# Kernel optimization log

Measured on AMD Instinct MI355X. Metric: run time of the kernel, lower is better.

## Reference

```python
import jax, jax.numpy as jnp
import numpy as np

TEMPERATURE = 0.07
NEG = -1e9  # finite stand-in for -inf; exp(-1e9) underflows to 0 in fp32, identical math


def setup_inputs() -> dict:
    key = jax.random.key(0)
    k1, k2 = jax.random.split(key)
    B, D = 8192, 128
    emb = jax.random.normal(k1, (B, D), dtype=jnp.float32)
    emb = emb / jnp.linalg.norm(emb, axis=1, keepdims=True)  # docstring: normalized embeddings
    labels = jax.random.randint(k2, (B,), 0, 2048, dtype=jnp.int64)
    return {"embeddings": emb, "labels": labels}


def reference(embeddings, labels):
    B = labels.shape[0]
    # [B, B] pairwise similarities / temperature
    sim = jnp.matmul(embeddings, embeddings.T) / TEMPERATURE
    eye = jnp.eye(B, dtype=bool)
    sim = jnp.where(eye, NEG, sim)  # mask self-similarity
    # positives: same outfit id, excluding self
    pos_mask = (labels[None, :] == labels[:, None]) & (~eye)
    # row-wise log-softmax (torch code does log_softmax over each row)
    log_probs = jax.nn.log_softmax(sim, axis=1)
    pos_count = jnp.sum(pos_mask, axis=1)  # [B]
    pos_sum = jnp.sum(jnp.where(pos_mask, log_probs, 0.0), axis=1)  # [B]
    has_pos = pos_count > 0
    row_mean = jnp.where(has_pos, pos_sum / jnp.maximum(pos_count, 1), 0.0)
    count = jnp.sum(has_pos)
    loss = -jnp.sum(row_mean) / jnp.maximum(count, 1)
    return loss
```

## Files before the change

### kernel.cpp

```cpp
#include <hip/hip_runtime.h>


#define BATCH 8192
#define DIMK  128
#define INV_T 14.285714285714286f
#define MSUB  14.285714285714286f
#define K1    20.609929155311264f
#define K2    20.609929155311264f

typedef short bf16x8 __attribute__((ext_vector_type(8)));
typedef float f32x4  __attribute__((ext_vector_type(4)));

__device__ __forceinline__ unsigned short f2bf_rne(float f) {
    unsigned u = __float_as_uint(f);
    u += 0x7FFFu + ((u >> 16) & 1u);
    return (unsigned short)(u >> 16);
}
__device__ __forceinline__ float bf2f(unsigned short b) {
    return __uint_as_float(((unsigned)b) << 16);
}

__global__ __launch_bounds__(256) void
prep_kernel(const float* __restrict__ emb, const int* __restrict__ labels,
            ushort* __restrict__ Ebf, float* __restrict__ gsum, int* __restrict__ gcnt,
            float4* __restrict__ zzero) {
    if (blockIdx.x < 1024) {
        int i = blockIdx.x * 256 + threadIdx.x;
        if (i < 67584) {
            float4 z = {0.f, 0.f, 0.f, 0.f};
            zzero[i] = z;
        }
        float4 v = ((const float4*)emb)[i];
        ushort4 o;
        o.x = f2bf_rne(v.x); o.y = f2bf_rne(v.y);
        o.z = f2bf_rne(v.z); o.w = f2bf_rne(v.w);
        ((ushort4*)Ebf)[i] = o;
    } else {
        __shared__ int labs[BATCH];
        const int tid = threadIdx.x;
#pragma unroll
        for (int it = 0; it < 8; ++it)
            ((int4*)labs)[it * 256 + tid] = ((const int4*)labels)[it * 256 + tid];
        __syncthreads();

        const int lane = tid & 63;
        const int wid  = tid >> 6;
        const int c    = (blockIdx.x - 1024) * 4 + wid;
        float2 acc = {0.f, 0.f};
        int cnt = 0;
        int nl = labs[lane];
        for (int j0 = 0; j0 < BATCH; j0 += 64) {
            int cur = nl;
            int nidx = j0 + 64 < BATCH ? j0 + 64 : 0;
            nl = labs[nidx + lane];
            unsigned long long m = __ballot(cur == c);
            cnt += __popcll(m);
            while (m) {
                int j = __ffsll(m) - 1;
                m &= m - 1;
                float2 v = *(const float2*)(emb + (size_t)(j0 + j) * DIMK + lane * 2);
                acc.x += v.x; acc.y += v.y;
            }
        }
        *(float2*)(gsum + (size_t)c * DIMK + lane * 2) = acc;
        if (lane == 0) gcnt[c] = cnt;
    }
}

__global__ __launch_bounds__(256) void
contrastive_main(const ushort* __restrict__ Ebf, float* __restrict__ zpartR,
                 float* __restrict__ zcol) {
    __shared__ __align__(16) ushort Bs[2048 * 8];
    __shared__ float cpart[4][256];
    const int tid  = threadIdx.x;
    const int lane = tid & 63;
    const int wid  = tid >> 6;
    const int quad = lane >> 4;
    const int l16  = lane & 15;

    int b = blockIdx.x >> 1;
    const int half = blockIdx.x & 1;
    int ti = 0;
    while (b >= 32 - ti) { b -= 32 - ti; ++ti; }
    const int tj = ti + b;
    const int row_base = ti * 256 + half * 128 + wid * 32;

    bf16x8 afrag[2][4];
#pragma unroll
    for (int mt = 0; mt < 2; ++mt)
#pragma unroll
        for (int kk = 0; kk < 4; ++kk)
            afrag[mt][kk] = *(const bf16x8*)(Ebf + (size_t)(row_base + mt * 16 + l16) * DIMK
                                             + kk * 32 + quad * 8);

    float zacc[8];
#pragma unroll
    for (int s = 0; s < 8; ++s) zacc[s] = 0.f;

#pragma unroll
    for (int phase = 0; phase < 2; ++phase) {
        const int col_base = tj * 256 + phase * 128;
        __syncthreads();
#pragma unroll
        for (int it = 0; it < 8; ++it) {
            int f   = it * 256 + tid;
            int col = f >> 4;
            int c   = f & 15;
            uint4 v = *(const uint4*)(Ebf + (size_t)(col_base + col) * DIMK + c * 8);
            *(uint4*)&Bs[((col >> 4) * 256 + c * 16 + ((col & 15) ^ c)) * 8] = v;
        }
        __syncthreads();

        for (int nt = 0; nt < 8; ++nt) {
            bf16x8 bfrag[4];
#pragma unroll
            for (int kk = 0; kk < 4; ++kk) {
                const int c2 = kk * 4 + quad;
                bfrag[kk] = *(const bf16x8*)&Bs[(nt * 256 + c2 * 16 + (l16 ^ c2)) * 8];
            }

            float csum = 0.f;
#pragma unroll
            for (int mt = 0; mt < 2; ++mt) {
                f32x4 c = {0.f, 0.f, 0.f, 0.f};
#pragma unroll
                for (int kk = 0; kk < 4; ++kk)
                    c = __builtin_amdgcn_mfma_f32_16x16x32_bf16(afrag[mt][kk], bfrag[kk], c, 0, 0, 0);
#pragma unroll
                for (int r = 0; r < 4; ++r) {
                    float e = __builtin_amdgcn_exp2f(__builtin_fmaf(c[r], K1, -K2));
                    zacc[mt * 4 + r] += e;
                    csum += e;
                }
            }
            csum += __shfl_xor(csum, 16, 64);
            csum += __shfl_xor(csum, 32, 64);
            if (quad == 0) cpart[wid][phase * 128 + nt * 16 + l16] = csum;
        }
    }

#pragma unroll
    for (int s = 0; s < 8; ++s) {
        float z = zacc[s];
#pragma unroll
        for (int m = 1; m <= 8; m <<= 1) z += __shfl_xor(z, m, 64);
        if (l16 == 0) {
            int row = row_base + (s >> 2) * 16 + quad * 4 + (s & 3);
            zpartR[(size_t)tj * BATCH + row] = z;
        }
    }

    __syncthreads();
    if (ti != tj) {
        float s = cpart[0][tid] + cpart[1][tid] + cpart[2][tid] + cpart[3][tid];
        atomicAdd(&zcol[tj * 256 + tid], s);
    }
}

__global__ __launch_bounds__(256) void
finalize1(const float* __restrict__ emb, const ushort* __restrict__ Ebf,
          const int* __restrict__ labels, const float* __restrict__ gsum,
          const int* __restrict__ gcnt, const float* __restrict__ zpartR,
          const float* __restrict__ zcol,
          float* __restrict__ bpart, int* __restrict__ bcnt) {
    __shared__ float sf[4];
    __shared__ int   si[4];
    const int lane = threadIdx.x & 63;
    const int wid  = threadIdx.x >> 6;

    float wsum = 0.f;
    int   wcnt = 0;
#pragma unroll
    for (int it = 0; it < 4; ++it) {
        const int r   = blockIdx.x * 16 + wid * 4 + it;
        const int lab = labels[r];
        const int P   = gcnt[lab] - 1;

        float2 ev = *(const float2*)(emb  + (size_t)r   * DIMK + lane * 2);
        float2 gv = *(const float2*)(gsum + (size_t)lab * DIMK + lane * 2);
        unsigned bb = *(const unsigned*)(Ebf + (size_t)r * DIMK + lane * 2);
        float b0 = bf2f((unsigned short)(bb & 0xFFFF));
        float b1 = bf2f((unsigned short)(bb >> 16));

        float dotg = ev.x * gv.x + ev.y * gv.y;
        float ssd  = ev.x * ev.x + ev.y * ev.y;
        float sdbf = b0 * b0 + b1 * b1;
        float Z = 0.f;
        if (lane < 32)       Z = zpartR[(size_t)lane * BATCH + r];
        else if (lane == 32) Z = zcol[r];

#pragma unroll
        for (int m = 1; m <= 32; m <<= 1) {
            dotg += __shfl_xor(dotg, m, 64);
            ssd  += __shfl_xor(ssd,  m, 64);
            sdbf += __shfl_xor(sdbf, m, 64);
            Z    += __shfl_xor(Z,    m, 64);
        }
        Z -= __builtin_amdgcn_exp2f(__builtin_fmaf(sdbf, K1, -K2));

        const bool has = (P > 0);
        wsum += has ? ((dotg - ssd) * INV_T / (float)P - MSUB - __logf(Z)) : 0.f;
        wcnt += has ? 1 : 0;
    }

    if (lane == 0) { sf[wid] = wsum; si[wid] = wcnt; }
    __syncthreads();
    if (threadIdx.x == 0) {
        bpart[blockIdx.x] = sf[0] + sf[1] + sf[2] + sf[3];
        bcnt [blockIdx.x] = si[0] + si[1] + si[2] + si[3];
    }
}

__global__ __launch_bounds__(256) void
finalize2(const float* __restrict__ bpart, const int* __restrict__ bcnt,
          float* __restrict__ out) {
    __shared__ float sf[4];
    __shared__ int   si[4];
    const int t = threadIdx.x;
    float v = 0.f; int c = 0;
#pragma unroll
    for (int k = 0; k < 2; ++k) {
        v += bpart[t + k * 256];
        c += bcnt [t + k * 256];
    }
#pragma unroll
    for (int m = 1; m <= 32; m <<= 1) {
        v += __shfl_xor(v, m, 64);
        c += __shfl_xor(c, m, 64);
    }
    if ((t & 63) == 0) { sf[t >> 6] = v; si[t >> 6] = c; }
    __syncthreads();
    if (t == 0) {
        float tot = sf[0] + sf[1] + sf[2] + sf[3];
        int cc = si[0] + si[1] + si[2] + si[3];
        out[0] = -tot / (float)(cc > 0 ? cc : 1);
    }
}

extern "C" void kernel_launch(void* const* d_in, const int* in_sizes, int n_in,
                              void* d_out, int out_size, void* d_ws, size_t ws_size,
                              hipStream_t stream) {
    const float* emb  = (const float*)d_in[0];
    const int* labels = (const int*)d_in[1];
    float* out        = (float*)d_out;

    char* ws = (char*)d_ws;
    ushort* Ebf    = (ushort*)ws;
    float*  zpartR = (float*)(ws + (2u << 20));
    float*  zcol   = (float*)(ws + (3u << 20));
    float*  gsum   = (float*)(ws + (4u << 20));
    int*    gcnt   = (int*)  (ws + (5u << 20));
    float*  bpart  = (float*)(ws + (5u << 20) + 8192);
    int*    bcnt   = (int*)  (ws + (5u << 20) + 16384);

    prep_kernel<<<1536, 256, 0, stream>>>(emb, labels, Ebf, gsum, gcnt, (float4*)zpartR);
    contrastive_main<<<1056, 256, 0, stream>>>(Ebf, zpartR, zcol);
    finalize1<<<512, 256, 0, stream>>>(emb, Ebf, labels, gsum, gcnt, zpartR, zcol, bpart, bcnt);
    finalize2<<<1, 256, 0, stream>>>(bpart, bcnt, out);
}
```

Before: 101.3 us.

## Double-buffer B tiles via direct global-to-LDS loads, use 32x32 MFMA, fuse final reduction

The main kernel now stages column chunks of 64 rows into two LDS buffers with global_load_lds and explicit vmcnt waits, so loading the next chunk overlaps MFMA and exp work on the current one. It also switches from 16x16x32 to 32x32x16 bf16 MFMA, which changes fragment layout and the row/column reduction mapping. The separate finalize2 launch is removed: the last block of finalize1, found with an atomic ticket, does the final sum. The risks are the hand-written waitcnt/barrier ordering and higher register use from the 16-wide accumulators.

```diff
diff --git a/kernel.cpp b/kernel.cpp
--- a/kernel.cpp
+++ b/kernel.cpp
@@ -9,7 +9,7 @@
 #define K2    20.609929155311264f
 
 typedef short bf16x8 __attribute__((ext_vector_type(8)));
-typedef float f32x4  __attribute__((ext_vector_type(4)));
+typedef float f32x16 __attribute__((ext_vector_type(16)));
 
 __device__ __forceinline__ unsigned short f2bf_rne(float f) {
     unsigned u = __float_as_uint(f);
@@ -20,11 +20,18 @@
     return __uint_as_float(((unsigned)b) << 16);
 }
 
+__device__ __forceinline__ void gload16(const ushort* g, ushort* l) {
+    __builtin_amdgcn_global_load_lds(
+        (const __attribute__((address_space(1))) void*)g,
+        (__attribute__((address_space(3))) void*)l, 16, 0, 0);
+}
+
 __global__ __launch_bounds__(256) void
 prep_kernel(const float* __restrict__ emb, const int* __restrict__ labels,
             ushort* __restrict__ Ebf, float* __restrict__ gsum, int* __restrict__ gcnt,
-            float4* __restrict__ zzero) {
+            float4* __restrict__ zzero, int* __restrict__ ticket) {
     if (blockIdx.x < 1024) {
+        if (blockIdx.x == 0 && threadIdx.x == 0) *ticket = 0;
         int i = blockIdx.x * 256 + threadIdx.x;
         if (i < 67584) {
             float4 z = {0.f, 0.f, 0.f, 0.f};
@@ -70,13 +77,13 @@
 __global__ __launch_bounds__(256) void
 contrastive_main(const ushort* __restrict__ Ebf, float* __restrict__ zpartR,
                  float* __restrict__ zcol) {
-    __shared__ __align__(16) ushort Bs[2048 * 8];
+    __shared__ __align__(16) ushort Bs[2][1024 * 8];
     __shared__ float cpart[4][256];
     const int tid  = threadIdx.x;
     const int lane = tid & 63;
     const int wid  = tid >> 6;
-    const int quad = lane >> 4;
-    const int l16  = lane & 15;
+    const int l32  = lane & 31;
+    const int hi   = lane >> 5;
 
     int b = blockIdx.x >> 1;
     const int half = blockIdx.x & 1;
@@ -84,68 +91,94 @@
     while (b >= 32 - ti) { b -= 32 - ti; ++ti; }
     const int tj = ti + b;
     const int row_base = ti * 256 + half * 128 + wid * 32;
-
-    bf16x8 afrag[2][4];
-#pragma unroll
-    for (int mt = 0; mt < 2; ++mt)
-#pragma unroll
-        for (int kk = 0; kk < 4; ++kk)
-            afrag[mt][kk] = *(const bf16x8*)(Ebf + (size_t)(row_base + mt * 16 + l16) * DIMK
-                                             + kk * 32 + quad * 8);
-
-    float zacc[8];
-#pragma unroll
-    for (int s = 0; s < 8; ++s) zacc[s] = 0.f;
-
-#pragma unroll
-    for (int phase = 0; phase < 2; ++phase) {
-        const int col_base = tj * 256 + phase * 128;
-        __syncthreads();
-#pragma unroll
-        for (int it = 0; it < 8; ++it) {
-            int f   = it * 256 + tid;
-            int col = f >> 4;
-            int c   = f & 15;
-            uint4 v = *(const uint4*)(Ebf + (size_t)(col_base + col) * DIMK + c * 8);
-            *(uint4*)&Bs[((col >> 4) * 256 + c * 16 + ((col & 15) ^ c)) * 8] = v;
-        }
-        __syncthreads();
-
-        for (int nt = 0; nt < 8; ++nt) {
-            bf16x8 bfrag[4];
-#pragma unroll
-            for (int kk = 0; kk < 4; ++kk) {
-                const int c2 = kk * 4 + quad;
-                bfrag[kk] = *(const bf16x8*)&Bs[(nt * 256 + c2 * 16 + (l16 ^ c2)) * 8];
-            }
-
-            float csum = 0.f;
-#pragma unroll
-            for (int mt = 0; mt < 2; ++mt) {
-                f32x4 c = {0.f, 0.f, 0.f, 0.f};
-#pragma unroll
-                for (int kk = 0; kk < 4; ++kk)
-                    c = __builtin_amdgcn_mfma_f32_16x16x32_bf16(afrag[mt][kk], bfrag[kk], c, 0, 0, 0);
-#pragma unroll
-                for (int r = 0; r < 4; ++r) {
-                    float e = __builtin_amdgcn_exp2f(__builtin_fmaf(c[r], K1, -K2));
-                    zacc[mt * 4 + r] += e;
-                    csum += e;
-                }
-            }
-            csum += __shfl_xor(csum, 16, 64);
-            csum += __shfl_xor(csum, 32, 64);
-            if (quad == 0) cpart[wid][phase * 128 + nt * 16 + l16] = csum;
-        }
-    }
-
-#pragma unroll
-    for (int s = 0; s < 8; ++s) {
-        float z = zacc[s];
-#pragma unroll
-        for (int m = 1; m <= 8; m <<= 1) z += __shfl_xor(z, m, 64);
-        if (l16 == 0) {
-            int row = row_base + (s >> 2) * 16 + quad * 4 + (s & 3);
+    const int col_tile = tj * 256;
+
+    bf16x8 afrag[8];
+#pragma unroll
+    for (int kk = 0; kk < 8; ++kk)
+        afrag[kk] = *(const bf16x8*)(Ebf + (size_t)(row_base + l32) * DIMK
+                                     + kk * 16 + hi * 8);
+
+    const ushort* gsrc[4];
+#pragma unroll
+    for (int it = 0; it < 4; ++it) {
+        const int u = it * 256 + tid;
+        const int g = u >> 8, c = (u >> 4) & 15, x = u & 15;
+        gsrc[it] = Ebf + (size_t)(col_tile + g * 16 + (x ^ c)) * DIMK + c * 8;
+    }
+
+    float zacc[16];
+#pragma unroll
+    for (int r = 0; r < 16; ++r) zacc[r] = 0.f;
+
+#define STAGE_CHUNK(K, BUF)                                                   \
+    {                                                                         \
+        _Pragma("unroll")                                                     \
+        for (int it = 0; it < 4; ++it)                                        \
+            gload16(gsrc[it] + (K) * 64 * DIMK,                               \
+                    &Bs[BUF][(it * 256 + wid * 64) * 8]);                     \
+    }
+
+#define COMPUTE_CHUNK(BUF, CB)                                                \
+    {                                                                         \
+        const ushort* bs = &Bs[BUF][0];                                       \
+        _Pragma("unroll")                                                     \
+        for (int nt = 0; nt < 2; ++nt) {                                      \
+            const int colL = nt * 32 + l32;                                   \
+            const int gp = (colL >> 4) * 256;                                 \
+            const int x0 = colL & 15;                                         \
+            bf16x8 bfrag[8];                                                  \
+            _Pragma("unroll")                                                 \
+            for (int kk = 0; kk < 8; ++kk) {                                  \
+                const int c = kk * 2 + hi;                                    \
+                bfrag[kk] = *(const bf16x8*)&bs[(size_t)(gp + c * 16 + (x0 ^ c)) * 8]; \
+            }                                                                 \
+            f32x16 acc;                                                       \
+            _Pragma("unroll")                                                 \
+            for (int r = 0; r < 16; ++r) acc[r] = 0.f;                        \
+            _Pragma("unroll")                                                 \
+            for (int kk = 0; kk < 8; ++kk)                                    \
+                acc = __builtin_amdgcn_mfma_f32_32x32x16_bf16(afrag[kk], bfrag[kk], acc, 0, 0, 0); \
+            float csum = 0.f;                                                 \
+            _Pragma("unroll")                                                 \
+            for (int r = 0; r < 16; ++r) {                                    \
+                float e = __builtin_amdgcn_exp2f(__builtin_fmaf(acc[r], K1, -K2)); \
+                zacc[r] += e; csum += e;                                      \
+            }                                                                 \
+            csum += __shfl_xor(csum, 32, 64);                                 \
+            if (hi == 0) cpart[wid][(CB) + nt * 32 + l32] = csum;             \
+        }                                                                     \
+    }
+
+    STAGE_CHUNK(0, 0);
+    STAGE_CHUNK(1, 1);
+    asm volatile("s_waitcnt vmcnt(4)" ::: "memory");
+    __builtin_amdgcn_s_barrier();
+    COMPUTE_CHUNK(0, 0);
+    __builtin_amdgcn_s_barrier();
+    STAGE_CHUNK(2, 0);
+    asm volatile("s_waitcnt vmcnt(4)" ::: "memory");
+    __builtin_amdgcn_s_barrier();
+    COMPUTE_CHUNK(1, 64);
+    __builtin_amdgcn_s_barrier();
+    STAGE_CHUNK(3, 1);
+    asm volatile("s_waitcnt vmcnt(4)" ::: "memory");
+    __builtin_amdgcn_s_barrier();
+    COMPUTE_CHUNK(0, 128);
+    asm volatile("s_waitcnt vmcnt(0)" ::: "memory");
+    __builtin_amdgcn_s_barrier();
+    COMPUTE_CHUNK(1, 192);
+
+#undef STAGE_CHUNK
+#undef COMPUTE_CHUNK
+
+#pragma unroll
+    for (int r = 0; r < 16; ++r) {
+        float z = zacc[r];
+#pragma unroll
+        for (int m = 1; m <= 16; m <<= 1) z += __shfl_xor(z, m, 64);
+        if (l32 == 0) {
+            int row = row_base + (r & 3) + 8 * (r >> 2) + 4 * hi;
             zpartR[(size_t)tj * BATCH + row] = z;
         }
     }
@@ -162,9 +195,11 @@
           const int* __restrict__ labels, const float* __restrict__ gsum,
           const int* __restrict__ gcnt, const float* __restrict__ zpartR,
           const float* __restrict__ zcol,
-          float* __restrict__ bpart, int* __restrict__ bcnt) {
+          float* __restrict__ bpart, int* __restrict__ bcnt,
+          int* __restrict__ ticket, float* __restrict__ out) {
     __shared__ float sf[4];
     __shared__ int   si[4];
+    __shared__ int   lastflag;
     const int lane = threadIdx.x & 63;
     const int wid  = threadIdx.x >> 6;
 
@@ -208,32 +243,27 @@
     if (threadIdx.x == 0) {
         bpart[blockIdx.x] = sf[0] + sf[1] + sf[2] + sf[3];
         bcnt [blockIdx.x] = si[0] + si[1] + si[2] + si[3];
-    }
-}
-
-__global__ __launch_bounds__(256) void
-finalize2(const float* __restrict__ bpart, const int* __restrict__ bcnt,
-          float* __restrict__ out) {
-    __shared__ float sf[4];
-    __shared__ int   si[4];
-    const int t = threadIdx.x;
-    float v = 0.f; int c = 0;
-#pragma unroll
-    for (int k = 0; k < 2; ++k) {
-        v += bpart[t + k * 256];
-        c += bcnt [t + k * 256];
-    }
-#pragma unroll
-    for (int m = 1; m <= 32; m <<= 1) {
-        v += __shfl_xor(v, m, 64);
-        c += __shfl_xor(c, m, 64);
-    }
-    if ((t & 63) == 0) { sf[t >> 6] = v; si[t >> 6] = c; }
+        __threadfence();
+        lastflag = (atomicAdd(ticket, 1) == (int)gridDim.x - 1);
+    }
     __syncthreads();
-    if (t == 0) {
-        float tot = sf[0] + sf[1] + sf[2] + sf[3];
-        int cc = si[0] + si[1] + si[2] + si[3];
-        out[0] = -tot / (float)(cc > 0 ? cc : 1);
+    if (lastflag) {
+        __threadfence();
+        const int t = threadIdx.x;
+        float v = bpart[t] + bpart[t + 256];
+        int   c = bcnt[t]  + bcnt[t + 256];
+#pragma unroll
+        for (int m = 1; m <= 32; m <<= 1) {
+            v += __shfl_xor(v, m, 64);
+            c += __shfl_xor(c, m, 64);
+        }
+        if ((t & 63) == 0) { sf[t >> 6] = v; si[t >> 6] = c; }
+        __syncthreads();
+        if (t == 0) {
+            float tot = sf[0] + sf[1] + sf[2] + sf[3];
+            int cc = si[0] + si[1] + si[2] + si[3];
+            out[0] = -tot / (float)(cc > 0 ? cc : 1);
+        }
     }
 }
 
@@ -252,9 +282,11 @@
     int*    gcnt   = (int*)  (ws + (5u << 20));
     float*  bpart  = (float*)(ws + (5u << 20) + 8192);
     int*    bcnt   = (int*)  (ws + (5u << 20) + 16384);
-
-    prep_kernel<<<1536, 256, 0, stream>>>(emb, labels, Ebf, gsum, gcnt, (float4*)zpartR);
+    int*    ticket = (int*)  (ws + (5u << 20) + 24576);
+
+    prep_kernel<<<1536, 256, 0, stream>>>(emb, labels, Ebf, gsum, gcnt,
+                                          (float4*)zpartR, ticket);
     contrastive_main<<<1056, 256, 0, stream>>>(Ebf, zpartR, zcol);
-    finalize1<<<512, 256, 0, stream>>>(emb, Ebf, labels, gsum, gcnt, zpartR, zcol, bpart, bcnt);
-    finalize2<<<1, 256, 0, stream>>>(bpart, bcnt, out);
-}
+    finalize1<<<512, 256, 0, stream>>>(emb, Ebf, labels, gsum, gcnt, zpartR, zcol,
+                                       bpart, bcnt, ticket, out);
+}
```

New measurement: 117.0 us. 1.16x slower.

## Fuse all four kernels into one cooperative persistent kernel with grid syncs

Applied to the files above, without the earlier changes.

Replaces the four separate launches (prep, main GEMM/exp tiles, finalize1, finalize2) with one cooperative kernel that uses grid.sync between phases. The final reduction is done by the last block, chosen with an atomic ticket. Group-sum computation is moved after the tile loop so it overlaps with tail blocks rather than running in prep. The aim is to remove kernel launch gaps and tail effects. In exchange it adds grid-wide barriers and limits the grid to the number of co-resident blocks, so blocks loop over tiles.

```diff
diff --git a/kernel.cpp b/kernel.cpp
--- a/kernel.cpp
+++ b/kernel.cpp
@@ -1,12 +1,16 @@
 #include <hip/hip_runtime.h>
-
-
-#define BATCH 8192
-#define DIMK  128
-#define INV_T 14.285714285714286f
-#define MSUB  14.285714285714286f
-#define K1    20.609929155311264f
-#define K2    20.609929155311264f
+#include <hip/hip_cooperative_groups.h>
+
+namespace cg = cooperative_groups;
+
+
+#define BATCH  8192
+#define DIMK   128
+#define INV_T  14.285714285714286f
+#define MSUB   14.285714285714286f
+#define K1     20.609929155311264f
+#define K2     20.609929155311264f
+#define NTILES 1056
 
 typedef short bf16x8 __attribute__((ext_vector_type(8)));
 typedef float f32x4  __attribute__((ext_vector_type(4)));
@@ -21,219 +25,230 @@
 }
 
 __global__ __launch_bounds__(256) void
-prep_kernel(const float* __restrict__ emb, const int* __restrict__ labels,
-            ushort* __restrict__ Ebf, float* __restrict__ gsum, int* __restrict__ gcnt,
-            float4* __restrict__ zzero) {
-    if (blockIdx.x < 1024) {
-        int i = blockIdx.x * 256 + threadIdx.x;
+contrastive_fused(const float* __restrict__ emb, const int* __restrict__ labels,
+                  ushort* __restrict__ Ebf, float* __restrict__ gsum,
+                  int* __restrict__ gcnt, float* __restrict__ zpartR,
+                  float* __restrict__ zcol, float* __restrict__ bpart,
+                  int* __restrict__ bcnt, int* __restrict__ ticket,
+                  float* __restrict__ out) {
+    __shared__ __align__(16) char smraw[36864];
+    cg::grid_group grid = cg::this_grid();
+    const int G    = gridDim.x;
+    const int bx   = blockIdx.x;
+    const int tid  = threadIdx.x;
+    const int lane = tid & 63;
+    const int wid  = tid >> 6;
+    const int quad = lane >> 4;
+    const int l16  = lane & 15;
+
+    if (bx == 0 && tid == 0) *ticket = 0;
+    for (int i = bx * 256 + tid; i < 262144; i += G * 256) {
         if (i < 67584) {
             float4 z = {0.f, 0.f, 0.f, 0.f};
-            zzero[i] = z;
+            ((float4*)zpartR)[i] = z;
         }
         float4 v = ((const float4*)emb)[i];
         ushort4 o;
         o.x = f2bf_rne(v.x); o.y = f2bf_rne(v.y);
         o.z = f2bf_rne(v.z); o.w = f2bf_rne(v.w);
         ((ushort4*)Ebf)[i] = o;
-    } else {
-        __shared__ int labs[BATCH];
-        const int tid = threadIdx.x;
-#pragma unroll
-        for (int it = 0; it < 8; ++it)
-            ((int4*)labs)[it * 256 + tid] = ((const int4*)labels)[it * 256 + tid];
+    }
+    grid.sync();
+
+    {
+        ushort* Bs = (ushort*)smraw;
+        float (*cpart)[256] = (float (*)[256])(smraw + 32768);
+
+        for (int tt = bx; tt < NTILES; tt += G) {
+            int b = tt >> 1;
+            const int half = tt & 1;
+            int ti = 0;
+            while (b >= 32 - ti) { b -= 32 - ti; ++ti; }
+            const int tj = ti + b;
+            const int row_base = ti * 256 + half * 128 + wid * 32;
+
+            bf16x8 afrag[2][4];
+#pragma unroll
+            for (int mt = 0; mt < 2; ++mt)
+#pragma unroll
+                for (int kk = 0; kk < 4; ++kk)
+                    afrag[mt][kk] = *(const bf16x8*)(Ebf
+                        + (size_t)(row_base + mt * 16 + l16) * DIMK
+                        + kk * 32 + quad * 8);
+
+            float zacc[8];
+#pragma unroll
+            for (int s = 0; s < 8; ++s) zacc[s] = 0.f;
+
+#pragma unroll
+            for (int phase = 0; phase < 2; ++phase) {
+                const int col_base = tj * 256 + phase * 128;
+                __syncthreads();
+#pragma unroll
+                for (int it = 0; it < 8; ++it) {
+                    int f   = it * 256 + tid;
+                    int col = f >> 4;
+                    int c   = f & 15;
+                    uint4 v = *(const uint4*)(Ebf
+                        + (size_t)(col_base + col) * DIMK + c * 8);
+                    *(uint4*)&Bs[((col >> 4) * 256 + c * 16 + ((col & 15) ^ c)) * 8] = v;
+                }
+                __syncthreads();
+
+                for (int nt = 0; nt < 8; ++nt) {
+                    bf16x8 bfrag[4];
+#pragma unroll
+                    for (int kk = 0; kk < 4; ++kk) {
+                        const int c2 = kk * 4 + quad;
+                        bfrag[kk] = *(const bf16x8*)&Bs[(nt * 256 + c2 * 16 + (l16 ^ c2)) * 8];
+                    }
+
+                    float csum = 0.f;
+#pragma unroll
+                    for (int mt = 0; mt < 2; ++mt) {
+                        f32x4 c = {0.f, 0.f, 0.f, 0.f};
+#pragma unroll
+                        for (int kk = 0; kk < 4; ++kk)
+                            c = __builtin_amdgcn_mfma_f32_16x16x32_bf16(
+                                    afrag[mt][kk], bfrag[kk], c, 0, 0, 0);
+#pragma unroll
+                        for (int r = 0; r < 4; ++r) {
+                            float e = __builtin_amdgcn_exp2f(__builtin_fmaf(c[r], K1, -K2));
+                            zacc[mt * 4 + r] += e;
+                            csum += e;
+                        }
+                    }
+                    csum += __shfl_xor(csum, 16, 64);
+                    csum += __shfl_xor(csum, 32, 64);
+                    if (quad == 0) cpart[wid][phase * 128 + nt * 16 + l16] = csum;
+                }
+            }
+
+#pragma unroll
+            for (int s = 0; s < 8; ++s) {
+                float z = zacc[s];
+#pragma unroll
+                for (int m = 1; m <= 8; m <<= 1) z += __shfl_xor(z, m, 64);
+                if (l16 == 0) {
+                    int row = row_base + (s >> 2) * 16 + quad * 4 + (s & 3);
+                    zpartR[(size_t)tj * BATCH + row] = z;
+                }
+            }
+
+            __syncthreads();
+            if (ti != tj) {
+                float s = cpart[0][tid] + cpart[1][tid] + cpart[2][tid] + cpart[3][tid];
+                atomicAdd(&zcol[tj * 256 + tid], s);
+            }
+        }
+    }
+
+    {
+        const int k = G - 1 - bx;
+        if (k * 4 < 2048) {
+            int* labs = (int*)smraw;
+            __syncthreads();
+#pragma unroll
+            for (int it = 0; it < 8; ++it)
+                ((int4*)labs)[it * 256 + tid] = ((const int4*)labels)[it * 256 + tid];
+            __syncthreads();
+
+            for (int c = k * 4 + wid; c < 2048; c += G * 4) {
+                float2 acc = {0.f, 0.f};
+                int cnt = 0;
+                int nl = labs[lane];
+                for (int j0 = 0; j0 < BATCH; j0 += 64) {
+                    int cur = nl;
+                    int nidx = j0 + 64 < BATCH ? j0 + 64 : 0;
+                    nl = labs[nidx + lane];
+                    unsigned long long m = __ballot(cur == c);
+                    cnt += __popcll(m);
+                    while (m) {
+                        int j = __ffsll(m) - 1;
+                        m &= m - 1;
+                        float2 v = *(const float2*)(emb + (size_t)(j0 + j) * DIMK + lane * 2);
+                        acc.x += v.x; acc.y += v.y;
+                    }
+                }
+                *(float2*)(gsum + (size_t)c * DIMK + lane * 2) = acc;
+                if (lane == 0) gcnt[c] = cnt;
+            }
+        }
+    }
+    grid.sync();
+
+    {
+        float* sf       = (float*)smraw;
+        int*   si       = (int*)(smraw + 64);
+        int*   lastflag = (int*)(smraw + 128);
+
+        for (int u = bx; u < 512; u += G) {
+            float wsum = 0.f;
+            int   wcnt = 0;
+#pragma unroll
+            for (int it = 0; it < 4; ++it) {
+                const int r   = u * 16 + wid * 4 + it;
+                const int lab = labels[r];
+                const int P   = gcnt[lab] - 1;
+
+                float2 ev = *(const float2*)(emb  + (size_t)r   * DIMK + lane * 2);
+                float2 gv = *(const float2*)(gsum + (size_t)lab * DIMK + lane * 2);
+                unsigned bb = *(const unsigned*)(Ebf + (size_t)r * DIMK + lane * 2);
+                float b0 = bf2f((unsigned short)(bb & 0xFFFF));
+                float b1 = bf2f((unsigned short)(bb >> 16));
+
+                float dotg = ev.x * gv.x + ev.y * gv.y;
+                float ssd  = ev.x * ev.x + ev.y * ev.y;
+                float sdbf = b0 * b0 + b1 * b1;
+                float Z = 0.f;
+                if (lane < 32)       Z = zpartR[(size_t)lane * BATCH + r];
+                else if (lane == 32) Z = zcol[r];
+
+#pragma unroll
+                for (int m = 1; m <= 32; m <<= 1) {
+                    dotg += __shfl_xor(dotg, m, 64);
+                    ssd  += __shfl_xor(ssd,  m, 64);
+                    sdbf += __shfl_xor(sdbf, m, 64);
+                    Z    += __shfl_xor(Z,    m, 64);
+                }
+                Z -= __builtin_amdgcn_exp2f(__builtin_fmaf(sdbf, K1, -K2));
+
+                const bool has = (P > 0);
+                wsum += has ? ((dotg - ssd) * INV_T / (float)P - MSUB - __logf(Z)) : 0.f;
+                wcnt += has ? 1 : 0;
+            }
+
+            if (lane == 0) { sf[wid] = wsum; si[wid] = wcnt; }
+            __syncthreads();
+            if (tid == 0) {
+                bpart[u] = sf[0] + sf[1] + sf[2] + sf[3];
+                bcnt [u] = si[0] + si[1] + si[2] + si[3];
+            }
+            __syncthreads();
+        }
+
+        __threadfence();
+        if (tid == 0)
+            *lastflag = (atomicAdd(ticket, 1) == G - 1) ? 1 : 0;
         __syncthreads();
-
-        const int lane = tid & 63;
-        const int wid  = tid >> 6;
-        const int c    = (blockIdx.x - 1024) * 4 + wid;
-        float2 acc = {0.f, 0.f};
-        int cnt = 0;
-        int nl = labs[lane];
-        for (int j0 = 0; j0 < BATCH; j0 += 64) {
-            int cur = nl;
-            int nidx = j0 + 64 < BATCH ? j0 + 64 : 0;
-            nl = labs[nidx + lane];
-            unsigned long long m = __ballot(cur == c);
-            cnt += __popcll(m);
-            while (m) {
-                int j = __ffsll(m) - 1;
-                m &= m - 1;
-                float2 v = *(const float2*)(emb + (size_t)(j0 + j) * DIMK + lane * 2);
-                acc.x += v.x; acc.y += v.y;
-            }
-        }
-        *(float2*)(gsum + (size_t)c * DIMK + lane * 2) = acc;
-        if (lane == 0) gcnt[c] = cnt;
-    }
-}
-
-__global__ __launch_bounds__(256) void
-contrastive_main(const ushort* __restrict__ Ebf, float* __restrict__ zpartR,
-                 float* __restrict__ zcol) {
-    __shared__ __align__(16) ushort Bs[2048 * 8];
-    __shared__ float cpart[4][256];
-    const int tid  = threadIdx.x;
-    const int lane = tid & 63;
-    const int wid  = tid >> 6;
-    const int quad = lane >> 4;
-    const int l16  = lane & 15;
-
-    int b = blockIdx.x >> 1;
-    const int half = blockIdx.x & 1;
-    int ti = 0;
-    while (b >= 32 - ti) { b -= 32 - ti; ++ti; }
-    const int tj = ti + b;
-    const int row_base = ti * 256 + half * 128 + wid * 32;
-
-    bf16x8 afrag[2][4];
-#pragma unroll
-    for (int mt = 0; mt < 2; ++mt)
-#pragma unroll
-        for (int kk = 0; kk < 4; ++kk)
-            afrag[mt][kk] = *(const bf16x8*)(Ebf + (size_t)(row_base + mt * 16 + l16) * DIMK
-                                             + kk * 32 + quad * 8);
-
-    float zacc[8];
-#pragma unroll
-    for (int s = 0; s < 8; ++s) zacc[s] = 0.f;
-
-#pragma unroll
-    for (int phase = 0; phase < 2; ++phase) {
-        const int col_base = tj * 256 + phase * 128;
-        __syncthreads();
-#pragma unroll
-        for (int it = 0; it < 8; ++it) {
-            int f   = it * 256 + tid;
-            int col = f >> 4;
-            int c   = f & 15;
-            uint4 v = *(const uint4*)(Ebf + (size_t)(col_base + col) * DIMK + c * 8);
-            *(uint4*)&Bs[((col >> 4) * 256 + c * 16 + ((col & 15) ^ c)) * 8] = v;
-        }
-        __syncthreads();
-
-        for (int nt = 0; nt < 8; ++nt) {
-            bf16x8 bfrag[4];
-#pragma unroll
-            for (int kk = 0; kk < 4; ++kk) {
-                const int c2 = kk * 4 + quad;
-                bfrag[kk] = *(const bf16x8*)&Bs[(nt * 256 + c2 * 16 + (l16 ^ c2)) * 8];
-            }
-
-            float csum = 0.f;
-#pragma unroll
-            for (int mt = 0; mt < 2; ++mt) {
-                f32x4 c = {0.f, 0.f, 0.f, 0.f};
-#pragma unroll
-                for (int kk = 0; kk < 4; ++kk)
-                    c = __builtin_amdgcn_mfma_f32_16x16x32_bf16(afrag[mt][kk], bfrag[kk], c, 0, 0, 0);
-#pragma unroll
-                for (int r = 0; r < 4; ++r) {
-                    float e = __builtin_amdgcn_exp2f(__builtin_fmaf(c[r], K1, -K2));
-                    zacc[mt * 4 + r] += e;
-                    csum += e;
-                }
-            }
-            csum += __shfl_xor(csum, 16, 64);
-            csum += __shfl_xor(csum, 32, 64);
-            if (quad == 0) cpart[wid][phase * 128 + nt * 16 + l16] = csum;
-        }
-    }
-
-#pragma unroll
-    for (int s = 0; s < 8; ++s) {
-        float z = zacc[s];
-#pragma unroll
-        for (int m = 1; m <= 8; m <<= 1) z += __shfl_xor(z, m, 64);
-        if (l16 == 0) {
-            int row = row_base + (s >> 2) * 16 + quad * 4 + (s & 3);
-            zpartR[(size_t)tj * BATCH + row] = z;
-        }
-    }
-
-    __syncthreads();
-    if (ti != tj) {
-        float s = cpart[0][tid] + cpart[1][tid] + cpart[2][tid] + cpart[3][tid];
-        atomicAdd(&zcol[tj * 256 + tid], s);
-    }
-}
-
-__global__ __launch_bounds__(256) void
-finalize1(const float* __restrict__ emb, const ushort* __restrict__ Ebf,
-          const int* __restrict__ labels, const float* __restrict__ gsum,
-          const int* __restrict__ gcnt, const float* __restrict__ zpartR,
-          const float* __restrict__ zcol,
-          float* __restrict__ bpart, int* __restrict__ bcnt) {
-    __shared__ float sf[4];
-    __shared__ int   si[4];
-    const int lane = threadIdx.x & 63;
-    const int wid  = threadIdx.x >> 6;
-
-    float wsum = 0.f;
-    int   wcnt = 0;
-#pragma unroll
-    for (int it = 0; it < 4; ++it) {
-        const int r   = blockIdx.x * 16 + wid * 4 + it;
-        const int lab = labels[r];
-        const int P   = gcnt[lab] - 1;
-
-        float2 ev = *(const float2*)(emb  + (size_t)r   * DIMK + lane * 2);
-        float2 gv = *(const float2*)(gsum + (size_t)lab * DIMK + lane * 2);
-        unsigned bb = *(const unsigned*)(Ebf + (size_t)r * DIMK + lane * 2);
-        float b0 = bf2f((unsigned short)(bb & 0xFFFF));
-        float b1 = bf2f((unsigned short)(bb >> 16));
-
-        float dotg = ev.x * gv.x + ev.y * gv.y;
-        float ssd  = ev.x * ev.x + ev.y * ev.y;
-        float sdbf = b0 * b0 + b1 * b1;
-        float Z = 0.f;
-        if (lane < 32)       Z = zpartR[(size_t)lane * BATCH + r];
-        else if (lane == 32) Z = zcol[r];
-
-#pragma unroll
-        for (int m = 1; m <= 32; m <<= 1) {
-            dotg += __shfl_xor(dotg, m, 64);
-            ssd  += __shfl_xor(ssd,  m, 64);
-            sdbf += __shfl_xor(sdbf, m, 64);
-            Z    += __shfl_xor(Z,    m, 64);
-        }
-        Z -= __builtin_amdgcn_exp2f(__builtin_fmaf(sdbf, K1, -K2));
-
-        const bool has = (P > 0);
-        wsum += has ? ((dotg - ssd) * INV_T / (float)P - MSUB - __logf(Z)) : 0.f;
-        wcnt += has ? 1 : 0;
-    }
-
-    if (lane == 0) { sf[wid] = wsum; si[wid] = wcnt; }
-    __syncthreads();
-    if (threadIdx.x == 0) {
-        bpart[blockIdx.x] = sf[0] + sf[1] + sf[2] + sf[3];
-        bcnt [blockIdx.x] = si[0] + si[1] + si[2] + si[3];
-    }
-}
-
-__global__ __launch_bounds__(256) void
-finalize2(const float* __restrict__ bpart, const int* __restrict__ bcnt,
-          float* __restrict__ out) {
-    __shared__ float sf[4];
-    __shared__ int   si[4];
-    const int t = threadIdx.x;
-    float v = 0.f; int c = 0;
-#pragma unroll
-    for (int k = 0; k < 2; ++k) {
-        v += bpart[t + k * 256];
-        c += bcnt [t + k * 256];
-    }
-#pragma unroll
-    for (int m = 1; m <= 32; m <<= 1) {
-        v += __shfl_xor(v, m, 64);
-        c += __shfl_xor(c, m, 64);
-    }
-    if ((t & 63) == 0) { sf[t >> 6] = v; si[t >> 6] = c; }
-    __syncthreads();
-    if (t == 0) {
-        float tot = sf[0] + sf[1] + sf[2] + sf[3];
-        int cc = si[0] + si[1] + si[2] + si[3];
-        out[0] = -tot / (float)(cc > 0 ? cc : 1);
+        if (*lastflag) {
+            __threadfence();
+            const int t = tid;
+            float v = bpart[t] + bpart[t + 256];
+            int   c = bcnt[t]  + bcnt[t + 256];
+#pragma unroll
+            for (int m = 1; m <= 32; m <<= 1) {
+                v += __shfl_xor(v, m, 64);
+                c += __shfl_xor(c, m, 64);
+            }
+            if ((t & 63) == 0) { sf[t >> 6] = v; si[t >> 6] = c; }
+            __syncthreads();
+            if (t == 0) {
+                float tot = sf[0] + sf[1] + sf[2] + sf[3];
+                int cc = si[0] + si[1] + si[2] + si[3];
+                out[0] = -tot / (float)(cc > 0 ? cc : 1);
+            }
+        }
     }
 }
 
@@ -252,9 +267,18 @@
     int*    gcnt   = (int*)  (ws + (5u << 20));
     float*  bpart  = (float*)(ws + (5u << 20) + 8192);
     int*    bcnt   = (int*)  (ws + (5u << 20) + 16384);
-
-    prep_kernel<<<1536, 256, 0, stream>>>(emb, labels, Ebf, gsum, gcnt, (float4*)zpartR);
-    contrastive_main<<<1056, 256, 0, stream>>>(Ebf, zpartR, zcol);
-    finalize1<<<512, 256, 0, stream>>>(emb, Ebf, labels, gsum, gcnt, zpartR, zcol, bpart, bcnt);
-    finalize2<<<1, 256, 0, stream>>>(bpart, bcnt, out);
-}
+    int*    ticket = (int*)  (ws + (5u << 20) + 24576);
+
+    int occ = 0;
+    if (hipOccupancyMaxActiveBlocksPerMultiprocessor(&occ, contrastive_fused, 256, 0)
+            != hipSuccess || occ < 1)
+        occ = 1;
+    int G = occ * 256;
+    if (G > NTILES) G = NTILES;
+
+    void* args[] = { (void*)&emb, (void*)&labels, (void*)&Ebf, (void*)&gsum,
+                     (void*)&gcnt, (void*)&zpartR, (void*)&zcol, (void*)&bpart,
+                     (void*)&bcnt, (void*)&ticket, (void*)&out };
+    hipLaunchCooperativeKernel((void*)contrastive_fused, dim3(G), dim3(256),
+                               args, 0, stream);
+}
```

Result: slower. 196.1 us (+93.7%).

## Load B fragments directly from global memory and skip zeroing unused partial sums

Applied to the files above, without the earlier changes.

The main kernel drops the LDS staging of the column tile, along with its two barriers per phase and the swizzled stores. Each wave now reads its B fragments straight from global memory (L2/L1-cached) in a single 16-iteration loop. The prep kernel only zeros the column-sum buffer instead of the whole partial-row buffer. finalize1 instead skips reading the lower-triangle partial entries that are never written. This removes LDS traffic and synchronisation, but every wave reloads the same B data from cache, which raises global/L1 load pressure.

```diff
diff --git a/kernel.cpp b/kernel.cpp
--- a/kernel.cpp
+++ b/kernel.cpp
@@ -23,12 +23,12 @@
 __global__ __launch_bounds__(256) void
 prep_kernel(const float* __restrict__ emb, const int* __restrict__ labels,
             ushort* __restrict__ Ebf, float* __restrict__ gsum, int* __restrict__ gcnt,
-            float4* __restrict__ zzero) {
+            float4* __restrict__ zcol4) {
     if (blockIdx.x < 1024) {
         int i = blockIdx.x * 256 + threadIdx.x;
-        if (i < 67584) {
+        if (i < 2048) {
             float4 z = {0.f, 0.f, 0.f, 0.f};
-            zzero[i] = z;
+            zcol4[i] = z;
         }
         float4 v = ((const float4*)emb)[i];
         ushort4 o;
@@ -70,7 +70,6 @@
 __global__ __launch_bounds__(256) void
 contrastive_main(const ushort* __restrict__ Ebf, float* __restrict__ zpartR,
                  float* __restrict__ zcol) {
-    __shared__ __align__(16) ushort Bs[2048 * 8];
     __shared__ float cpart[4][256];
     const int tid  = threadIdx.x;
     const int lane = tid & 63;
@@ -97,46 +96,32 @@
 #pragma unroll
     for (int s = 0; s < 8; ++s) zacc[s] = 0.f;
 
-#pragma unroll
-    for (int phase = 0; phase < 2; ++phase) {
-        const int col_base = tj * 256 + phase * 128;
-        __syncthreads();
-#pragma unroll
-        for (int it = 0; it < 8; ++it) {
-            int f   = it * 256 + tid;
-            int col = f >> 4;
-            int c   = f & 15;
-            uint4 v = *(const uint4*)(Ebf + (size_t)(col_base + col) * DIMK + c * 8);
-            *(uint4*)&Bs[((col >> 4) * 256 + c * 16 + ((col & 15) ^ c)) * 8] = v;
-        }
-        __syncthreads();
-
-        for (int nt = 0; nt < 8; ++nt) {
-            bf16x8 bfrag[4];
-#pragma unroll
-            for (int kk = 0; kk < 4; ++kk) {
-                const int c2 = kk * 4 + quad;
-                bfrag[kk] = *(const bf16x8*)&Bs[(nt * 256 + c2 * 16 + (l16 ^ c2)) * 8];
+    const ushort* bbase = Ebf + (size_t)(tj * 256 + l16) * DIMK + quad * 8;
+
+#pragma unroll 2
+    for (int nt = 0; nt < 16; ++nt) {
+        bf16x8 bfrag[4];
+#pragma unroll
+        for (int kk = 0; kk < 4; ++kk)
+            bfrag[kk] = *(const bf16x8*)(bbase + nt * (16 * DIMK) + kk * 32);
+
+        float csum = 0.f;
+#pragma unroll
+        for (int mt = 0; mt < 2; ++mt) {
+            f32x4 c = {0.f, 0.f, 0.f, 0.f};
+#pragma unroll
+            for (int kk = 0; kk < 4; ++kk)
+                c = __builtin_amdgcn_mfma_f32_16x16x32_bf16(afrag[mt][kk], bfrag[kk], c, 0, 0, 0);
+#pragma unroll
+            for (int r = 0; r < 4; ++r) {
+                float e = __builtin_amdgcn_exp2f(__builtin_fmaf(c[r], K1, -K2));
+                zacc[mt * 4 + r] += e;
+                csum += e;
             }
-
-            float csum = 0.f;
-#pragma unroll
-            for (int mt = 0; mt < 2; ++mt) {
-                f32x4 c = {0.f, 0.f, 0.f, 0.f};
-#pragma unroll
-                for (int kk = 0; kk < 4; ++kk)
-                    c = __builtin_amdgcn_mfma_f32_16x16x32_bf16(afrag[mt][kk], bfrag[kk], c, 0, 0, 0);
-#pragma unroll
-                for (int r = 0; r < 4; ++r) {
-                    float e = __builtin_amdgcn_exp2f(__builtin_fmaf(c[r], K1, -K2));
-                    zacc[mt * 4 + r] += e;
-                    csum += e;
-                }
-            }
-            csum += __shfl_xor(csum, 16, 64);
-            csum += __shfl_xor(csum, 32, 64);
-            if (quad == 0) cpart[wid][phase * 128 + nt * 16 + l16] = csum;
-        }
+        }
+        csum += __shfl_xor(csum, 16, 64);
+        csum += __shfl_xor(csum, 32, 64);
+        if (quad == 0) cpart[wid][nt * 16 + l16] = csum;
     }
 
 #pragma unroll
@@ -175,6 +160,7 @@
         const int r   = blockIdx.x * 16 + wid * 4 + it;
         const int lab = labels[r];
         const int P   = gcnt[lab] - 1;
+        const int tp  = r >> 8;
 
         float2 ev = *(const float2*)(emb  + (size_t)r   * DIMK + lane * 2);
         float2 gv = *(const float2*)(gsum + (size_t)lab * DIMK + lane * 2);
@@ -186,8 +172,11 @@
         float ssd  = ev.x * ev.x + ev.y * ev.y;
         float sdbf = b0 * b0 + b1 * b1;
         float Z = 0.f;
-        if (lane < 32)       Z = zpartR[(size_t)lane * BATCH + r];
-        else if (lane == 32) Z = zcol[r];
+        if (lane < 32) {
+            if (lane >= tp) Z = zpartR[(size_t)lane * BATCH + r];
+        } else if (lane == 32) {
+            Z = zcol[r];
+        }
 
 #pragma unroll
         for (int m = 1; m <= 32; m <<= 1) {
@@ -253,8 +242,10 @@
     float*  bpart  = (float*)(ws + (5u << 20) + 8192);
     int*    bcnt   = (int*)  (ws + (5u << 20) + 16384);
 
-    prep_kernel<<<1536, 256, 0, stream>>>(emb, labels, Ebf, gsum, gcnt, (float4*)zpartR);
+    prep_kernel<<<1536, 256, 0, stream>>>(emb, labels, Ebf, gsum, gcnt,
+                                          (float4*)zcol);
     contrastive_main<<<1056, 256, 0, stream>>>(Ebf, zpartR, zcol);
-    finalize1<<<512, 256, 0, stream>>>(emb, Ebf, labels, gsum, gcnt, zpartR, zcol, bpart, bcnt);
+    finalize1<<<512, 256, 0, stream>>>(emb, Ebf, labels, gsum, gcnt, zpartR, zcol,
+                                       bpart, bcnt);
     finalize2<<<1, 256, 0, stream>>>(bpart, bcnt, out);
 }
```

After: 117.3 us. 1.16x slower.
